# Kernel optimization log

Measured on AMD Instinct MI355X. Metric: run time of the kernel, lower is better.

## Reference

```python
import jax, jax.numpy as jnp
from jax import lax
import numpy as np

TAU = 1.0          # epoch buffer = 0 -> tau_init * decay^0 = 1.0
NEG = -1.0e9
K_HOP = 2
MAX_CLUSTERS = 16
SIZE_MAX = 8
SIZE_MIN = 1
THRESH = 0.95
EPS = 1e-8


def _gumbel_hard(key, logits, m):
    # torch: logits*mask + (1-mask)*-1e9; gumbel noise; softmax; straight-through one-hot
    mf = m.astype(logits.dtype)
    ml = logits * mf + (1.0 - mf) * NEG
    u = jax.random.uniform(key, logits.shape, dtype=logits.dtype)
    g = -jnp.log(-jnp.log(u + EPS) + EPS)
    soft = jax.nn.softmax((ml + g) / TAU, axis=-1)
    idx = jnp.argmax(soft, axis=-1)
    hard = jax.nn.one_hot(idx, logits.shape[-1], dtype=logits.dtype)
    return hard + soft - lax.stop_gradient(soft), idx


def _k_hop(adj, seed_idx, m):
    # vectorized BFS via masked bmm, fixed K_HOP iterations
    N = adj.shape[1]
    seed = jax.nn.one_hot(seed_idx, N, dtype=bool)
    reach, cur = seed, seed
    for _ in range(K_HOP):
        nb = (jnp.einsum('bn,bnm->bm', cur.astype(adj.dtype), adj) > 0) & m
        new = nb & (~reach)
        reach = reach | nb
        cur = new
    return reach


def _topk_gumbel(key, logits, k, m):
    # iterative hard gumbel selection of up to k nodes per batch (k: [B] int)
    sel = jnp.zeros_like(logits)
    remaining = m
    for step in range(SIZE_MAX - SIZE_MIN):
        key, sk = jax.random.split(key)
        active = (step < k) & remaining.any(-1)
        step_mask = remaining & active[:, None]
        s, _ = _gumbel_hard(sk, logits, step_mask)
        sel = sel + s * active[:, None].astype(sel.dtype)
        remaining = remaining & ~(lax.stop_gradient(s) > 0.5)
    return sel


def _gru_seq(hist, h0, Wih, Whh, bih, bhh):
    # torch nn.GRU cell math, scan over time; hist [B,T,D], h0 [B,H]
    H = h0.shape[-1]
    def step(h, xt):
        gi = xt @ Wih.T + bih
        gh = h @ Whh.T + bhh
        r = jax.nn.sigmoid(gi[:, :H] + gh[:, :H])
        z = jax.nn.sigmoid(gi[:, H:2 * H] + gh[:, H:2 * H])
        n = jnp.tanh(gi[:, 2 * H:] + r * gh[:, 2 * H:])
        return (1.0 - z) * n + z * h, None
    h_final, _ = lax.scan(step, h0, jnp.swapaxes(hist, 0, 1))
    return h_final


def _forward(x, adj, mask, sel_w1, sel_b1, sel_w2, sel_b2,
             size_w1, size_b1, size_w2, size_b2,
             gru_wih, gru_whh, gru_bih, gru_bhh, init_w, init_b):
    B, N, D = x.shape
    H = init_w.shape[0]
    maskf = mask.astype(x.dtype)
    total = maskf.sum(-1)                                   # [B]
    x_mean = (x * maskf[:, :, None]).sum(1) / (total[:, None] + EPS)
    ctx_hidden = x_mean @ init_w.T + init_b                 # [B,H]
    global_ctx = ctx_hidden
    assignment = jnp.zeros((B, N, MAX_CLUSTERS), x.dtype)
    assigned = jnp.zeros((B, N), bool)
    history = []
    key = jax.random.key(42)
    size_range = jnp.arange(SIZE_MAX - SIZE_MIN + 1)
    for c in range(MAX_CLUSTERS):
        # gradient-safe early termination: mask contributions instead of breaking
        pct = assignment.sum((1, 2)) / (total + EPS)
        active = (pct < THRESH) & (total > 0)
        avail = mask & (~assigned)
        # selection MLP on [x, context]
        sel_in = jnp.concatenate(
            [x, jnp.broadcast_to(global_ctx[:, None, :], (B, N, H))], -1)
        h1 = jax.nn.relu(sel_in @ sel_w1.T + sel_b1)
        logits = (h1 @ sel_w2.T + sel_b2)[..., 0]           # [B,N]
        key, k1, k2, k3 = jax.random.split(key, 4)
        seed_sel, seed_idx = _gumbel_hard(k1, logits, avail)
        seed_feat = jnp.einsum('bn,bnd->bd', seed_sel, x)
        khop = _k_hop(adj, seed_idx, avail)
        candidates = khop & avail
        max_possible = jnp.minimum(candidates.sum(-1), SIZE_MAX)
        # cluster-size prediction
        size_in = jnp.concatenate(
            [seed_feat, global_ctx, max_possible.astype(x.dtype)[:, None]], -1)
        sh = jax.nn.relu(size_in @ size_w1.T + size_b1)
        size_logits = sh @ size_w2.T + size_b2              # [B,8]
        valid_ranges = jnp.clip(max_possible - SIZE_MIN + 1, 1, size_logits.shape[-1])
        range_mask = size_range[None, :] < valid_ranges[:, None]
        size_sel, _ = _gumbel_hard(k2, size_logits, range_mask)
        sizes = jnp.argmax(size_sel, -1) + SIZE_MIN         # [B]
        seed_oh = jax.nn.one_hot(seed_idx, N, dtype=bool)
        extra = _topk_gumbel(k3, logits, sizes - 1, candidates & (~seed_oh))
        cluster_sel = (seed_sel + extra) * active.astype(x.dtype)[:, None]
        assignment = assignment.at[:, :, c].set(cluster_sel)
        assigned = assigned | (lax.stop_gradient(cluster_sel) > 0.5)
        # gradient-safe cluster embedding (mean over selected nodes)
        csize = jnp.maximum(lax.stop_gradient(cluster_sel).sum(-1), 1.0)
        emb = jnp.einsum('bn,bnd->bd', cluster_sel, x) / csize[:, None]
        emb = emb * active.astype(x.dtype)[:, None]
        history.append(emb)
        # update_context_safe: rerun GRU on full history from current hidden
        hist = jnp.stack(history, 1)                        # [B,t+1,D]
        ctx_hidden = _gru_seq(hist, ctx_hidden, gru_wih, gru_whh, gru_bih, gru_bhh)
        global_ctx = ctx_hidden
    return assignment


def setup_inputs() -> dict:
    key = jax.random.key(0)
    ks = jax.random.split(key, 16)
    B, N, D, H = 32, 512, 128, 128
    x = jax.random.normal(ks[0], (B, N, D), jnp.float32)
    a = (jax.random.uniform(ks[1], (B, N, N)) < 0.02).astype(jnp.float32)
    adj = jnp.maximum(a, jnp.swapaxes(a, 1, 2))             # symmetric binary contacts
    mask = jnp.ones((B, N), bool)
    s = 0.05
    p = lambda k, sh: jax.random.normal(k, sh, jnp.float32) * s
    return dict(
        x=x, adj=adj, mask=mask,
        sel_w1=p(ks[2], (H, D + H)), sel_b1=p(ks[3], (H,)),
        sel_w2=p(ks[4], (1, H)), sel_b2=p(ks[5], (1,)),
        size_w1=p(ks[6], (H, D + H + 1)), size_b1=p(ks[7], (H,)),
        size_w2=p(ks[8], (SIZE_MAX, H)), size_b2=p(ks[9], (SIZE_MAX,)),
        gru_wih=p(ks[10], (3 * H, D)), gru_whh=p(ks[11], (3 * H, H)),
        gru_bih=p(ks[12], (3 * H,)), gru_bhh=p(ks[13], (3 * H,)),
        init_w=p(ks[14], (H, D)), init_b=p(ks[15], (H,)))


def reference(x, adj, mask, sel_w1, sel_b1, sel_w2, sel_b2,
              size_w1, size_b1, size_w2, size_b2,
              gru_wih, gru_whh, gru_bih, gru_bhh, init_w, init_b):
    return _forward(x, adj, mask, sel_w1, sel_b1, sel_w2, sel_b2,
                    size_w1, size_b1, size_w2, size_b2,
                    gru_wih, gru_whh, gru_bih, gru_bhh, init_w, init_b)
```

## Files before the change

kernel.cpp:

```cpp
#include <hip/hip_runtime.h>
#include <stdint.h>


#define NBATCH 32
#define NNODE  512
#define NDIM   128
#define NHID   128
#define NCLUS  16
#define NEGV   (-1.0e9f)
#define EPSF   (1e-8f)

struct KeyPack {
  uint32_t k1[NCLUS][2];
  uint32_t k2[NCLUS][2];
  uint32_t sk[NCLUS][7][2];
};

__host__ __device__ inline void tf2x32(uint32_t k0, uint32_t k1,
                                       uint32_t x0, uint32_t x1,
                                       uint32_t& o0, uint32_t& o1) {
  uint32_t k2 = k0 ^ k1 ^ 0x1BD11BDAu;
#define TFR(r) { x0 += x1; x1 = (x1 << (r)) | (x1 >> (32 - (r))); x1 ^= x0; }
  x0 += k0; x1 += k1;
  TFR(13) TFR(15) TFR(26) TFR(6)
  x0 += k1; x1 += k2 + 1u;
  TFR(17) TFR(29) TFR(16) TFR(24)
  x0 += k2; x1 += k0 + 2u;
  TFR(13) TFR(15) TFR(26) TFR(6)
  x0 += k0; x1 += k1 + 3u;
  TFR(17) TFR(29) TFR(16) TFR(24)
  x0 += k1; x1 += k2 + 4u;
  TFR(13) TFR(15) TFR(26) TFR(6)
  x0 += k2; x1 += k0 + 5u;
#undef TFR
  o0 = x0; o1 = x1;
}

__device__ __forceinline__ float jax_uniform(uint32_t k0, uint32_t k1, uint32_t j) {
  uint32_t a, b;
  tf2x32(k0, k1, 0u, j, a, b);
  uint32_t bits = a ^ b;
  return __uint_as_float((bits >> 9) | 0x3F800000u) - 1.0f;
}

__device__ __forceinline__ float gumb(float u) {
  return -logf(-logf(u + EPSF) + EPSF);
}

__device__ __forceinline__ float sigmf(float v) { return 1.0f / (1.0f + expf(-v)); }

__device__ __forceinline__ int block_argmax512(float v, int idx,
                                               float* rv, int* ri, int* res) {
  const int lane = threadIdx.x & 63;
  const int wid  = threadIdx.x >> 6;
#pragma unroll
  for (int off = 32; off > 0; off >>= 1) {
    float ov = __shfl_down(v, off);
    int   oi = __shfl_down(idx, off);
    if (ov > v || (ov == v && oi < idx)) { v = ov; idx = oi; }
  }
  if (lane == 0) { rv[wid] = v; ri[wid] = idx; }
  __syncthreads();
  if (threadIdx.x < 64) {
    float bv = (lane < 8) ? rv[lane] : -3.4e38f;
    int   bi = (lane < 8) ? ri[lane] : 0x7fffffff;
#pragma unroll
    for (int off = 4; off > 0; off >>= 1) {
      float ov = __shfl_down(bv, off);
      int   oi = __shfl_down(bi, off);
      if (ov > bv || (ov == bv && oi < bi)) { bv = ov; bi = oi; }
    }
    if (lane == 0) *res = bi;
  }
  __syncthreads();
  return *res;
}


__global__ void k_transpose(const float* __restrict__ gwih,
                            const float* __restrict__ selw1, const float* __restrict__ szw1,
                            const float* __restrict__ initw,
                            float* __restrict__ WihT,
                            float* __restrict__ W1cT, float* __restrict__ szW1T,
                            float* __restrict__ initWT) {
  int t = blockIdx.x * blockDim.x + threadIdx.x;
  if (t < 128 * 384) {
    int j = t / 384, i = t % 384;
    WihT[t] = gwih[i * 128 + j];
  }
  if (t < 128 * 128) {
    int j = t >> 7, hh = t & 127;
    W1cT[t]   = selw1[hh * 256 + 128 + j];
    initWT[t] = initw[hh * 128 + j];
  }
  if (t < 257 * 128) {
    int j = t >> 7, i = t & 127;
    szW1T[t] = szw1[i * 257 + j];
  }
}

__global__ void k_adjbits(const float* __restrict__ adj, uint8_t* __restrict__ adjb8) {
  int t = blockIdx.x * blockDim.x + threadIdx.x;
  if (t >= NBATCH * NNODE * 64) return;
  const float4* p = (const float4*)adj + (size_t)t * 2;
  float4 a = p[0], b = p[1];
  uint32_t m = (a.x > 0.f ? 1u : 0u) | (a.y > 0.f ? 2u : 0u)
             | (a.z > 0.f ? 4u : 0u) | (a.w > 0.f ? 8u : 0u)
             | (b.x > 0.f ? 16u : 0u) | (b.y > 0.f ? 32u : 0u)
             | (b.z > 0.f ? 64u : 0u) | (b.w > 0.f ? 128u : 0u);
  adjb8[t] = (uint8_t)m;
}

__global__ __launch_bounds__(512)
void k_xw1(const float* __restrict__ x, const float* __restrict__ selw1,
           float* __restrict__ xw1T) {
  const int b = blockIdx.x >> 3;
  const int n0 = (blockIdx.x & 7) * 64;
  __shared__ float xs[64][NDIM + 1];
  for (int i = threadIdx.x; i < 64 * NDIM; i += 512) {
    int n = i >> 7, d = i & 127;
    xs[n][d] = x[((size_t)b * NNODE + n0 + n) * NDIM + d];
  }
  __syncthreads();
  for (int p = threadIdx.x; p < 64 * NHID; p += 512) {
    int h = p >> 6, n = p & 63;
    const float* wr = selw1 + h * 256;
    float a0 = 0.f, a1 = 0.f, a2 = 0.f, a3 = 0.f;
#pragma unroll 8
    for (int d = 0; d < NDIM; d += 4) {
      a0 = fmaf(xs[n][d + 0], wr[d + 0], a0);
      a1 = fmaf(xs[n][d + 1], wr[d + 1], a1);
      a2 = fmaf(xs[n][d + 2], wr[d + 2], a2);
      a3 = fmaf(xs[n][d + 3], wr[d + 3], a3);
    }
    xw1T[((size_t)b * NHID + h) * NNODE + n0 + n] = (a0 + a1) + (a2 + a3);
  }
}


__global__
__attribute__((amdgpu_flat_work_group_size(512, 512), amdgpu_waves_per_eu(1, 2)))
void k_main(const float* __restrict__ x,
            const float* __restrict__ selb1, const float* __restrict__ selw2,
            const float* __restrict__ selb2,
            const float* __restrict__ szb1, const float* __restrict__ szw2,
            const float* __restrict__ szb2,
            const float* __restrict__ gwhh,
            const float* __restrict__ gbih, const float* __restrict__ gbhh,
            const float* __restrict__ initb,
            const float* __restrict__ xw1T, const uint32_t* __restrict__ adjb,
            const float* __restrict__ WihT,
            const float* __restrict__ W1cT, const float* __restrict__ szW1T,
            const float* __restrict__ initWT,
            float* __restrict__ out, KeyPack kp)
{
  const int b = blockIdx.x;
  const int t = threadIdx.x;
  const int lane = t & 63, wid = t >> 6;

  __shared__ __align__(16) float ctxb[2][NHID];
  __shared__ __align__(16) float ctxterm[NHID];
  __shared__ __align__(16) float gic[NCLUS][3 * NHID];
  __shared__ __align__(16) float cat256[2 * NHID];
  __shared__ __align__(16) float embs[NDIM];
  __shared__ __align__(16) float h1s[NHID];
  __shared__ __align__(16) float xm[NHID];
  __shared__ __align__(16) float part4[1536];
  __shared__ __align__(16) float selw2s[NHID];
  __shared__ __align__(16) float szw2s[8 * NHID];
  __shared__ float slog[8];
  __shared__ float rv[8];
  __shared__ int   ri[8];
  __shared__ int   ibox[4];
  __shared__ uint32_t curm[16];
  __shared__ uint32_t selm[16];

  const int tau1 = 512 + t, tau2 = 1024 + t;
  const int q0 = (t    >= 384) ? 1 : 0;  const int i0 = (t    >= 384) ? t    - 384 : t;
  const int q1 = (tau1 >= 768) ? 2 : 1;  const int i1 = (tau1 >= 768) ? tau1 - 768 : tau1 - 384;
  const int q2 = (tau2 >= 1152) ? 3 : 2; const int i2 = (tau2 >= 1152) ? tau2 - 1152 : tau2 - 768;

  float4 wc0[8], wc1[8], wc2[8];
  {
    const float4* w0 = (const float4*)(gwhh + (size_t)i0 * 128 + q0 * 32);
    const float4* w1 = (const float4*)(gwhh + (size_t)i1 * 128 + q1 * 32);
    const float4* w2 = (const float4*)(gwhh + (size_t)i2 * 128 + q2 * 32);
#pragma unroll
    for (int k4 = 0; k4 < 8; k4++) { wc0[k4] = w0[k4]; wc1[k4] = w1[k4]; wc2[k4] = w2[k4]; }
  }

  if (t < NHID) selw2s[t] = selw2[t];
  for (int i = t; i < 8 * NHID; i += 512) szw2s[i] = szw2[i];
  const float selb2_r = selb2[0];
  const float szb2_r  = szb2[wid];
  const float selb1_r = (t < NHID) ? selb1[t] : 0.f;
  const float szb1_r  = (t < NHID) ? szb1[t] : 0.f;
  const float szw1mp_r = (t < NHID) ? szW1T[256 * NHID + t] : 0.f;
  const float gbih_r  = (t < 384) ? gbih[t] : 0.f;
  float gb0 = 0.f, gb1 = 0.f, gb2 = 0.f;
  if (t < NHID) { gb0 = gbhh[t]; gb1 = gbhh[NHID + t]; gb2 = gbhh[2 * NHID + t]; }

  {
    const int j = t & 127, p = t >> 7;
    const float* xp = x + ((size_t)b * NNODE + p * 128) * NDIM + j;
    float a0 = 0.f, a1 = 0.f, a2 = 0.f, a3 = 0.f;
#pragma unroll 4
    for (int n = 0; n < 128; n += 4) {
      a0 += xp[(size_t)(n + 0) * NDIM];
      a1 += xp[(size_t)(n + 1) * NDIM];
      a2 += xp[(size_t)(n + 2) * NDIM];
      a3 += xp[(size_t)(n + 3) * NDIM];
    }
    part4[p * 128 + j] = (a0 + a1) + (a2 + a3);
  }
  __syncthreads();
  if (t < NHID) xm[t] = (part4[t] + part4[128 + t] + part4[256 + t] + part4[384 + t]) * (1.0f / 512.0f);
  __syncthreads();
  if (t < NHID) {
    float a = initb[t];
    const float4* x4 = (const float4*)xm;
#pragma unroll 8
    for (int j4 = 0; j4 < 32; j4++) {
      float4 v = x4[j4];
      int j = 4 * j4;
      a = fmaf(v.x, initWT[(j + 0) * NHID + t], a);
      a = fmaf(v.y, initWT[(j + 1) * NHID + t], a);
      a = fmaf(v.z, initWT[(j + 2) * NHID + t], a);
      a = fmaf(v.w, initWT[(j + 3) * NHID + t], a);
    }
    ctxb[0][t] = a;
  }
  __syncthreads();

  int cur = 0;
  bool assigned = false;
  uint32_t selbits = 0u;

  for (int c = 0; c < NCLUS; c++) {
    {
      const int hh = t & 127, p = t >> 7;
      const float4* c4 = (const float4*)(ctxb[cur] + p * 32);
      float a0 = 0.f, a1 = 0.f, a2 = 0.f, a3 = 0.f;
#pragma unroll
      for (int j4 = 0; j4 < 8; j4++) {
        float4 cv = c4[j4];
        int j = p * 32 + j4 * 4;
        a0 = fmaf(cv.x, W1cT[(j + 0) * NHID + hh], a0);
        a1 = fmaf(cv.y, W1cT[(j + 1) * NHID + hh], a1);
        a2 = fmaf(cv.z, W1cT[(j + 2) * NHID + hh], a2);
        a3 = fmaf(cv.w, W1cT[(j + 3) * NHID + hh], a3);
      }
      part4[p * 128 + hh] = (a0 + a1) + (a2 + a3);
    }
    __syncthreads();
    if (t < NHID) ctxterm[t] = selb1_r + part4[t] + part4[128 + t] + part4[256 + t] + part4[384 + t];
    __syncthreads();

    float myLogit;
    {
      float acc0 = selb2_r, acc1 = 0.f, acc2 = 0.f, acc3 = 0.f;
      const float* xp = xw1T + (size_t)b * NHID * NNODE + t;
      const float4* ct4 = (const float4*)ctxterm;
      const float4* w24 = (const float4*)selw2s;
#pragma unroll 8
      for (int h4 = 0; h4 < 32; h4++) {
        float4 cv = ct4[h4], wv = w24[h4];
        int h = h4 * 4;
        acc0 = fmaf(fmaxf(xp[(size_t)(h + 0) * NNODE] + cv.x, 0.f), wv.x, acc0);
        acc1 = fmaf(fmaxf(xp[(size_t)(h + 1) * NNODE] + cv.y, 0.f), wv.y, acc1);
        acc2 = fmaf(fmaxf(xp[(size_t)(h + 2) * NNODE] + cv.z, 0.f), wv.z, acc2);
        acc3 = fmaf(fmaxf(xp[(size_t)(h + 3) * NNODE] + cv.w, 0.f), wv.w, acc3);
      }
      myLogit = (acc0 + acc1) + (acc2 + acc3);
    }

    const bool avail = !assigned;
    float z = (avail ? myLogit : NEGV)
            + gumb(jax_uniform(kp.k1[c][0], kp.k1[c][1], (uint32_t)(b * NNODE + t)));
    const int seed = block_argmax512(z, t, rv, ri, &ibox[0]);

    bool reach = (t == seed);
    if (t < 16) curm[t] = ((seed >> 5) == t) ? (1u << (seed & 31)) : 0u;
    __syncthreads();
    const uint32_t* arow = adjb + ((size_t)b * NNODE + t) * 16;
    for (int hop = 0; hop < 2; hop++) {
      uint32_t mr = 0u;
#pragma unroll
      for (int w = 0; w < 16; w++) mr |= arow[w] & curm[w];
      const bool nb = (mr != 0u) && avail;
      const bool nw = nb && !reach;
      reach = reach || nb;
      __syncthreads();
      unsigned long long bal = __ballot(nw);
      if (lane == 0) { curm[wid * 2] = (uint32_t)bal; curm[wid * 2 + 1] = (uint32_t)(bal >> 32); }
      __syncthreads();
    }
    const bool cand = reach && avail;
    {
      unsigned long long cb = __ballot(cand);
      if (lane == 0) ri[wid] = __popcll(cb);
      __syncthreads();
      if (t == 0) { int s = 0; for (int w = 0; w < 8; w++) s += ri[w]; ibox[1] = s; }
      __syncthreads();
    }
    const int candcnt = ibox[1];
    const int mp = min(candcnt, 8);

    if (t < NHID) {
      cat256[t]        = x[((size_t)b * NNODE + seed) * NDIM + t];
      cat256[NHID + t] = ctxb[cur][t];
    }
    __syncthreads();
    {
      const int hh = t & 127, p = t >> 7;
      const float4* c4 = (const float4*)(cat256 + p * 64);
      float a0 = 0.f, a1 = 0.f, a2 = 0.f, a3 = 0.f;
#pragma unroll
      for (int j4 = 0; j4 < 16; j4++) {
        float4 cv = c4[j4];
        int j = p * 64 + j4 * 4;
        a0 = fmaf(cv.x, szW1T[(j + 0) * NHID + hh], a0);
        a1 = fmaf(cv.y, szW1T[(j + 1) * NHID + hh], a1);
        a2 = fmaf(cv.z, szW1T[(j + 2) * NHID + hh], a2);
        a3 = fmaf(cv.w, szW1T[(j + 3) * NHID + hh], a3);
      }
      part4[p * 128 + hh] = (a0 + a1) + (a2 + a3);
    }
    __syncthreads();
    if (t < NHID) {
      float a = szb1_r + ((part4[t] + part4[128 + t]) + (part4[256 + t] + part4[384 + t]))
              + (float)mp * szw1mp_r;
      h1s[t] = fmaxf(a, 0.f);
    }
    __syncthreads();
    {
      float a = h1s[lane] * szw2s[wid * NHID + lane]
              + h1s[64 + lane] * szw2s[wid * NHID + 64 + lane];
#pragma unroll
      for (int off = 32; off > 0; off >>= 1) a += __shfl_down(a, off);
      if (lane == 0) {
        float g2 = gumb(jax_uniform(kp.k2[c][0], kp.k2[c][1], (uint32_t)(b * 8 + wid)));
        slog[wid] = ((wid < mp) ? (a + szb2_r) : NEGV) + g2;
      }
    }
    __syncthreads();
    if (t == 0) {
      float bv = slog[0]; int bi = 0;
      for (int q = 1; q < 8; q++) if (slog[q] > bv) { bv = slog[q]; bi = q; }
      ibox[2] = bi;
    }
    __syncthreads();
    const int kextra = ibox[2];

    bool sel = (t == seed);
    bool remaining = cand && !sel;
    int remcnt = candcnt - 1;
    int selcnt = 1;
    for (int s = 0; s < kextra; s++) {
      if (remcnt <= 0) break;
      float z3 = (remaining ? myLogit : NEGV)
               + gumb(jax_uniform(kp.sk[c][s][0], kp.sk[c][s][1], (uint32_t)(b * NNODE + t)));
      const int pick = block_argmax512(z3, t, rv, ri, &ibox[3]);
      if (t == pick) { sel = true; remaining = false; }
      remcnt--; selcnt++;
    }

    if (sel) selbits |= (1u << c);
    assigned = assigned || sel;

    {
      unsigned long long sb = __ballot(sel);
      if (lane == 0) { selm[wid * 2] = (uint32_t)sb; selm[wid * 2 + 1] = (uint32_t)(sb >> 32); }
    }
    __syncthreads();
    if (t < NDIM) {
      float a = 0.f;
      for (int w = 0; w < 16; w++) {
        uint32_t mwd = selm[w];
        while (mwd) {
          int bit = __ffs(mwd) - 1;
          mwd &= mwd - 1;
          a += x[((size_t)b * NNODE + (w * 32 + bit)) * NDIM + t];
        }
      }
      embs[t] = a / (float)selcnt;
    }
    __syncthreads();

    {
      const float4* e4 = (const float4*)embs;
      float pa, pb;
#define GI_TASK(Q, I)                                                     \
      pa = 0.f; pb = 0.f;                                                 \
      _Pragma("unroll")                                                   \
      for (int k4 = 0; k4 < 8; k4++) {                                    \
        float4 ev = e4[(Q) * 8 + k4];                                     \
        const float* wp = WihT + (size_t)((Q) * 32 + 4 * k4) * 384 + (I); \
        pa = fmaf(ev.x, wp[0],    pa);                                    \
        pb = fmaf(ev.y, wp[384],  pb);                                    \
        pa = fmaf(ev.z, wp[768],  pa);                                    \
        pb = fmaf(ev.w, wp[1152], pb);                                    \
      }                                                                   \
      part4[(Q) * 384 + (I)] = pa + pb;
      GI_TASK(q0, i0)
      GI_TASK(q1, i1)
      GI_TASK(q2, i2)
#undef GI_TASK
    }
    __syncthreads();
    if (t < 384)
      gic[c][t] = gbih_r + ((part4[t] + part4[384 + t]) + (part4[768 + t] + part4[1152 + t]));
    __syncthreads();

    for (int tt = 0; tt <= c; tt++) {
      {
        const float4* c4 = (const float4*)ctxb[cur];
        float pa, pb;
#define GH_TASK(WC, Q, I)                                   \
        pa = 0.f; pb = 0.f;                                 \
        _Pragma("unroll")                                   \
        for (int k4 = 0; k4 < 8; k4++) {                    \
          float4 w = WC[k4];                                \
          float4 v = c4[(Q) * 8 + k4];                      \
          pa = fmaf(w.x, v.x, pa);                          \
          pb = fmaf(w.y, v.y, pb);                          \
          pa = fmaf(w.z, v.z, pa);                          \
          pb = fmaf(w.w, v.w, pb);                          \
        }                                                   \
        part4[(Q) * 384 + (I)] = pa + pb;
        GH_TASK(wc0, q0, i0)
        GH_TASK(wc1, q1, i1)
        GH_TASK(wc2, q2, i2)
#undef GH_TASK
      }
      __syncthreads();
      if (t < NHID) {
        float ghr = (part4[t]       + part4[384 + t])  + (part4[768 + t]  + part4[1152 + t]);
        float ghz = (part4[128 + t] + part4[512 + t])  + (part4[896 + t]  + part4[1280 + t]);
        float ghn = (part4[256 + t] + part4[640 + t])  + (part4[1024 + t] + part4[1408 + t]);
        const float* gi = gic[tt];
        float r  = sigmf(gi[t] + ghr + gb0);
        float zz = sigmf(gi[NHID + t] + ghz + gb1);
        float nn = tanhf(gi[2 * NHID + t] + r * (ghn + gb2));
        ctxb[cur ^ 1][t] = (1.f - zz) * nn + zz * ctxb[cur][t];
      }
      __syncthreads();
      cur ^= 1;
    }
  }

  float4* o4 = (float4*)(out + ((size_t)b * NNODE + t) * NCLUS);
#pragma unroll
  for (int q = 0; q < 4; q++) {
    float4 v;
    v.x = (selbits >> (4 * q + 0)) & 1u ? 1.f : 0.f;
    v.y = (selbits >> (4 * q + 1)) & 1u ? 1.f : 0.f;
    v.z = (selbits >> (4 * q + 2)) & 1u ? 1.f : 0.f;
    v.w = (selbits >> (4 * q + 3)) & 1u ? 1.f : 0.f;
    o4[q] = v;
  }
}


extern "C" void kernel_launch(void* const* d_in, const int* in_sizes, int n_in,
                              void* d_out, int out_size, void* d_ws, size_t ws_size,
                              hipStream_t stream) {
  (void)in_sizes; (void)n_in; (void)out_size; (void)ws_size;

  const float* x     = (const float*)d_in[0];
  const float* adj   = (const float*)d_in[1];
  const float* selw1 = (const float*)d_in[3];
  const float* selb1 = (const float*)d_in[4];
  const float* selw2 = (const float*)d_in[5];
  const float* selb2 = (const float*)d_in[6];
  const float* szw1  = (const float*)d_in[7];
  const float* szb1  = (const float*)d_in[8];
  const float* szw2  = (const float*)d_in[9];
  const float* szb2  = (const float*)d_in[10];
  const float* gwih  = (const float*)d_in[11];
  const float* gwhh  = (const float*)d_in[12];
  const float* gbih  = (const float*)d_in[13];
  const float* gbhh  = (const float*)d_in[14];
  const float* initw = (const float*)d_in[15];
  const float* initb = (const float*)d_in[16];
  float* out = (float*)d_out;

  float*    xw1T   = (float*)d_ws;
  uint32_t* adjb   = (uint32_t*)(xw1T + (size_t)NBATCH * NHID * NNODE);
  float*    WihT   = (float*)(adjb + (size_t)NBATCH * NNODE * 16);
  float*    W1cT   = WihT + 128 * 384;
  float*    szW1T  = W1cT + 128 * 128;
  float*    initWT = szW1T + 257 * 128;

  KeyPack kp;
  uint32_t kk0 = 0u, kk1 = 42u;
  for (int c = 0; c < NCLUS; c++) {
    uint32_t nk0, nk1, t0, t1, u0, u1;
    tf2x32(kk0, kk1, 0u, 0u, nk0, nk1);
    tf2x32(kk0, kk1, 0u, 1u, kp.k1[c][0], kp.k1[c][1]);
    tf2x32(kk0, kk1, 0u, 2u, kp.k2[c][0], kp.k2[c][1]);
    tf2x32(kk0, kk1, 0u, 3u, t0, t1);
    for (int s = 0; s < 7; s++) {
      tf2x32(t0, t1, 0u, 1u, kp.sk[c][s][0], kp.sk[c][s][1]);
      tf2x32(t0, t1, 0u, 0u, u0, u1);
      t0 = u0; t1 = u1;
    }
    kk0 = nk0; kk1 = nk1;
  }

  k_transpose<<<192, 256, 0, stream>>>(gwih, selw1, szw1, initw,
                                       WihT, W1cT, szW1T, initWT);
  k_adjbits<<<(NBATCH * NNODE * 64) / 256, 256, 0, stream>>>(adj, (uint8_t*)adjb);
  k_xw1<<<NBATCH * 8, 512, 0, stream>>>(x, selw1, xw1T);
  k_main<<<NBATCH, 512, 0, stream>>>(x, selb1, selw2, selb2, szb1, szw2, szb2,
                                     gwhh, gbih, gbhh, initb, xw1T, adjb,
                                     WihT, W1cT, szW1T, initWT, out, kp);
}
```

Baseline: 767.8 us.

## Stream GRU weights from a float4-interleaved global layout instead of register caching

The GRU recurrent weights were previously held in registers per thread (96 floats per thread). They are now rewritten by the transpose kernel into a float4-interleaved layout and streamed from global memory/L2 in each recurrent step. Each wave handles a 16-column slice and writes to an 8-way partial buffer. The input-gate matvec uses the same layout and helper macro. The aim is to relieve register pressure and use coalesced loads, at the cost of re-reading weights from cache every GRU step and a larger shared partial-sum buffer.

```diff
diff --git a/kernel.cpp b/kernel.cpp
--- a/kernel.cpp
+++ b/kernel.cpp
@@ -78,15 +78,19 @@
 
 
 __global__ void k_transpose(const float* __restrict__ gwih,
+                            const float* __restrict__ gwhh,
                             const float* __restrict__ selw1, const float* __restrict__ szw1,
                             const float* __restrict__ initw,
-                            float* __restrict__ WihT,
+                            float4* __restrict__ Wi3, float4* __restrict__ W3,
                             float* __restrict__ W1cT, float* __restrict__ szW1T,
                             float* __restrict__ initWT) {
   int t = blockIdx.x * blockDim.x + threadIdx.x;
-  if (t < 128 * 384) {
-    int j = t / 384, i = t % 384;
-    WihT[t] = gwih[i * 128 + j];
+  if (t < 32 * 384) {
+    int i = t % 384, j4 = t / 384;
+    const float* si = gwih + i * 128 + j4 * 4;
+    Wi3[t] = make_float4(si[0], si[1], si[2], si[3]);
+    const float* sh = gwhh + i * 128 + j4 * 4;
+    W3[t]  = make_float4(sh[0], sh[1], sh[2], sh[3]);
   }
   if (t < 128 * 128) {
     int j = t >> 7, hh = t & 127;
@@ -138,18 +142,37 @@
 }
 
 
-__global__
-__attribute__((amdgpu_flat_work_group_size(512, 512), amdgpu_waves_per_eu(1, 2)))
+#define MV384_PARTIALS(WP4, V4, PART)                                        \
+  {                                                                          \
+    const float4 cv0 = (V4)[wid * 4 + 0], cv1 = (V4)[wid * 4 + 1];           \
+    const float4 cv2 = (V4)[wid * 4 + 2], cv3 = (V4)[wid * 4 + 3];           \
+    _Pragma("unroll")                                                        \
+    for (int m = 0; m < 6; m++) {                                            \
+      const int row = lane + 64 * m;                                         \
+      float4 w0 = (WP4)[row], w1 = (WP4)[384 + row];                         \
+      float4 w2 = (WP4)[768 + row], w3v = (WP4)[1152 + row];                 \
+      float pa = w0.x * cv0.x, pb = w0.y * cv0.y;                            \
+      pa = fmaf(w0.z, cv0.z, pa);  pb = fmaf(w0.w, cv0.w, pb);               \
+      pa = fmaf(w1.x, cv1.x, pa);  pb = fmaf(w1.y, cv1.y, pb);               \
+      pa = fmaf(w1.z, cv1.z, pa);  pb = fmaf(w1.w, cv1.w, pb);               \
+      pa = fmaf(w2.x, cv2.x, pa);  pb = fmaf(w2.y, cv2.y, pb);               \
+      pa = fmaf(w2.z, cv2.z, pa);  pb = fmaf(w2.w, cv2.w, pb);               \
+      pa = fmaf(w3v.x, cv3.x, pa); pb = fmaf(w3v.y, cv3.y, pb);              \
+      pa = fmaf(w3v.z, cv3.z, pa); pb = fmaf(w3v.w, cv3.w, pb);              \
+      (PART)[wid * 384 + row] = pa + pb;                                     \
+    }                                                                        \
+  }
+
+__global__ __launch_bounds__(512)
 void k_main(const float* __restrict__ x,
             const float* __restrict__ selb1, const float* __restrict__ selw2,
             const float* __restrict__ selb2,
             const float* __restrict__ szb1, const float* __restrict__ szw2,
             const float* __restrict__ szb2,
-            const float* __restrict__ gwhh,
             const float* __restrict__ gbih, const float* __restrict__ gbhh,
             const float* __restrict__ initb,
             const float* __restrict__ xw1T, const uint32_t* __restrict__ adjb,
-            const float* __restrict__ WihT,
+            const float4* __restrict__ Wi3, const float4* __restrict__ W3,
             const float* __restrict__ W1cT, const float* __restrict__ szW1T,
             const float* __restrict__ initWT,
             float* __restrict__ out, KeyPack kp)
@@ -165,7 +188,7 @@
   __shared__ __align__(16) float embs[NDIM];
   __shared__ __align__(16) float h1s[NHID];
   __shared__ __align__(16) float xm[NHID];
-  __shared__ __align__(16) float part4[1536];
+  __shared__ __align__(16) float part[8 * 384];
   __shared__ __align__(16) float selw2s[NHID];
   __shared__ __align__(16) float szw2s[8 * NHID];
   __shared__ float slog[8];
@@ -174,20 +197,6 @@
   __shared__ int   ibox[4];
   __shared__ uint32_t curm[16];
   __shared__ uint32_t selm[16];
-
-  const int tau1 = 512 + t, tau2 = 1024 + t;
-  const int q0 = (t    >= 384) ? 1 : 0;  const int i0 = (t    >= 384) ? t    - 384 : t;
-  const int q1 = (tau1 >= 768) ? 2 : 1;  const int i1 = (tau1 >= 768) ? tau1 - 768 : tau1 - 384;
-  const int q2 = (tau2 >= 1152) ? 3 : 2; const int i2 = (tau2 >= 1152) ? tau2 - 1152 : tau2 - 768;
-
-  float4 wc0[8], wc1[8], wc2[8];
-  {
-    const float4* w0 = (const float4*)(gwhh + (size_t)i0 * 128 + q0 * 32);
-    const float4* w1 = (const float4*)(gwhh + (size_t)i1 * 128 + q1 * 32);
-    const float4* w2 = (const float4*)(gwhh + (size_t)i2 * 128 + q2 * 32);
-#pragma unroll
-    for (int k4 = 0; k4 < 8; k4++) { wc0[k4] = w0[k4]; wc1[k4] = w1[k4]; wc2[k4] = w2[k4]; }
-  }
 
   if (t < NHID) selw2s[t] = selw2[t];
   for (int i = t; i < 8 * NHID; i += 512) szw2s[i] = szw2[i];
@@ -211,10 +220,10 @@
       a2 += xp[(size_t)(n + 2) * NDIM];
       a3 += xp[(size_t)(n + 3) * NDIM];
     }
-    part4[p * 128 + j] = (a0 + a1) + (a2 + a3);
+    part[p * 128 + j] = (a0 + a1) + (a2 + a3);
   }
   __syncthreads();
-  if (t < NHID) xm[t] = (part4[t] + part4[128 + t] + part4[256 + t] + part4[384 + t]) * (1.0f / 512.0f);
+  if (t < NHID) xm[t] = (part[t] + part[128 + t] + part[256 + t] + part[384 + t]) * (1.0f / 512.0f);
   __syncthreads();
   if (t < NHID) {
     float a = initb[t];
@@ -250,10 +259,10 @@
         a2 = fmaf(cv.z, W1cT[(j + 2) * NHID + hh], a2);
         a3 = fmaf(cv.w, W1cT[(j + 3) * NHID + hh], a3);
       }
-      part4[p * 128 + hh] = (a0 + a1) + (a2 + a3);
-    }
-    __syncthreads();
-    if (t < NHID) ctxterm[t] = selb1_r + part4[t] + part4[128 + t] + part4[256 + t] + part4[384 + t];
+      part[p * 128 + hh] = (a0 + a1) + (a2 + a3);
+    }
+    __syncthreads();
+    if (t < NHID) ctxterm[t] = selb1_r + part[t] + part[128 + t] + part[256 + t] + part[384 + t];
     __syncthreads();
 
     float myLogit;
@@ -324,11 +333,11 @@
         a2 = fmaf(cv.z, szW1T[(j + 2) * NHID + hh], a2);
         a3 = fmaf(cv.w, szW1T[(j + 3) * NHID + hh], a3);
       }
-      part4[p * 128 + hh] = (a0 + a1) + (a2 + a3);
+      part[p * 128 + hh] = (a0 + a1) + (a2 + a3);
     }
     __syncthreads();
     if (t < NHID) {
-      float a = szb1_r + ((part4[t] + part4[128 + t]) + (part4[256 + t] + part4[384 + t]))
+      float a = szb1_r + ((part[t] + part[128 + t]) + (part[256 + t] + part[384 + t]))
               + (float)mp * szw1mp_r;
       h1s[t] = fmaxf(a, 0.f);
     }
@@ -388,56 +397,36 @@
     __syncthreads();
 
     {
+      uintptr_t wp = (uintptr_t)Wi3;
+      asm volatile("" : "+s"(wp));
+      const float4* wi = (const float4*)wp + (size_t)wid * 4 * 384;
       const float4* e4 = (const float4*)embs;
-      float pa, pb;
-#define GI_TASK(Q, I)                                                     \
-      pa = 0.f; pb = 0.f;                                                 \
-      _Pragma("unroll")                                                   \
-      for (int k4 = 0; k4 < 8; k4++) {                                    \
-        float4 ev = e4[(Q) * 8 + k4];                                     \
-        const float* wp = WihT + (size_t)((Q) * 32 + 4 * k4) * 384 + (I); \
-        pa = fmaf(ev.x, wp[0],    pa);                                    \
-        pb = fmaf(ev.y, wp[384],  pb);                                    \
-        pa = fmaf(ev.z, wp[768],  pa);                                    \
-        pb = fmaf(ev.w, wp[1152], pb);                                    \
-      }                                                                   \
-      part4[(Q) * 384 + (I)] = pa + pb;
-      GI_TASK(q0, i0)
-      GI_TASK(q1, i1)
-      GI_TASK(q2, i2)
-#undef GI_TASK
-    }
-    __syncthreads();
-    if (t < 384)
-      gic[c][t] = gbih_r + ((part4[t] + part4[384 + t]) + (part4[768 + t] + part4[1152 + t]));
+      MV384_PARTIALS(wi, e4, part)
+    }
+    __syncthreads();
+    if (t < 384) {
+      gic[c][t] = gbih_r
+                + (((part[t] + part[384 + t]) + (part[768 + t] + part[1152 + t]))
+                 + ((part[1536 + t] + part[1920 + t]) + (part[2304 + t] + part[2688 + t])));
+    }
     __syncthreads();
 
     for (int tt = 0; tt <= c; tt++) {
       {
+        uintptr_t wp = (uintptr_t)W3;
+        asm volatile("" : "+s"(wp));
+        const float4* w3p = (const float4*)wp + (size_t)wid * 4 * 384;
         const float4* c4 = (const float4*)ctxb[cur];
-        float pa, pb;
-#define GH_TASK(WC, Q, I)                                   \
-        pa = 0.f; pb = 0.f;                                 \
-        _Pragma("unroll")                                   \
-        for (int k4 = 0; k4 < 8; k4++) {                    \
-          float4 w = WC[k4];                                \
-          float4 v = c4[(Q) * 8 + k4];                      \
-          pa = fmaf(w.x, v.x, pa);                          \
-          pb = fmaf(w.y, v.y, pb);                          \
-          pa = fmaf(w.z, v.z, pa);                          \
-          pb = fmaf(w.w, v.w, pb);                          \
-        }                                                   \
-        part4[(Q) * 384 + (I)] = pa + pb;
-        GH_TASK(wc0, q0, i0)
-        GH_TASK(wc1, q1, i1)
-        GH_TASK(wc2, q2, i2)
-#undef GH_TASK
+        MV384_PARTIALS(w3p, c4, part)
       }
       __syncthreads();
       if (t < NHID) {
-        float ghr = (part4[t]       + part4[384 + t])  + (part4[768 + t]  + part4[1152 + t]);
-        float ghz = (part4[128 + t] + part4[512 + t])  + (part4[896 + t]  + part4[1280 + t]);
-        float ghn = (part4[256 + t] + part4[640 + t])  + (part4[1024 + t] + part4[1408 + t]);
+        float ghr = ((part[t]        + part[384 + t])  + (part[768 + t]  + part[1152 + t]))
+                  + ((part[1536 + t] + part[1920 + t]) + (part[2304 + t] + part[2688 + t]));
+        float ghz = ((part[128 + t]  + part[512 + t])  + (part[896 + t]  + part[1280 + t]))
+                  + ((part[1664 + t] + part[2048 + t]) + (part[2432 + t] + part[2816 + t]));
+        float ghn = ((part[256 + t]  + part[640 + t])  + (part[1024 + t] + part[1408 + t]))
+                  + ((part[1792 + t] + part[2176 + t]) + (part[2560 + t] + part[2944 + t]));
         const float* gi = gic[tt];
         float r  = sigmf(gi[t] + ghr + gb0);
         float zz = sigmf(gi[NHID + t] + ghz + gb1);
@@ -487,8 +476,9 @@
 
   float*    xw1T   = (float*)d_ws;
   uint32_t* adjb   = (uint32_t*)(xw1T + (size_t)NBATCH * NHID * NNODE);
-  float*    WihT   = (float*)(adjb + (size_t)NBATCH * NNODE * 16);
-  float*    W1cT   = WihT + 128 * 384;
+  float*    Wi3    = (float*)(adjb + (size_t)NBATCH * NNODE * 16);
+  float*    W3     = Wi3 + 384 * 128;
+  float*    W1cT   = W3 + 384 * 128;
   float*    szW1T  = W1cT + 128 * 128;
   float*    initWT = szW1T + 257 * 128;
 
@@ -508,11 +498,13 @@
     kk0 = nk0; kk1 = nk1;
   }
 
-  k_transpose<<<192, 256, 0, stream>>>(gwih, selw1, szw1, initw,
-                                       WihT, W1cT, szW1T, initWT);
+  k_transpose<<<192, 256, 0, stream>>>(gwih, gwhh, selw1, szw1, initw,
+                                       (float4*)Wi3, (float4*)W3,
+                                       W1cT, szW1T, initWT);
   k_adjbits<<<(NBATCH * NNODE * 64) / 256, 256, 0, stream>>>(adj, (uint8_t*)adjb);
   k_xw1<<<NBATCH * 8, 512, 0, stream>>>(x, selw1, xw1T);
   k_main<<<NBATCH, 512, 0, stream>>>(x, selb1, selw2, selb2, szb1, szw2, szb2,
-                                     gwhh, gbih, gbhh, initb, xw1T, adjb,
-                                     WihT, W1cT, szW1T, initWT, out, kp);
-}
+                                     gbih, gbhh, initb, xw1T, adjb,
+                                     (const float4*)Wi3, (const float4*)W3,
+                                     W1cT, szW1T, initWT, out, kp);
+}
```

After: 740.7 us. -3.5%, faster.
